# Kernel tuning notes

Hardware: AMD Instinct MI355X
Metric: run time of the kernel (lower is better)

The kernel has to match this reference:

```python
import jax, jax.numpy as jnp
import numpy as np

B, S, D, H = 32, 512, 256, 4
DK = D // H  # d_k = d_q = d_v = 64


def setup_inputs() -> dict:
    key = jax.random.key(0)
    ks = jax.random.split(key, 10)
    lim_qk = np.sqrt(6.0 / (D + DK))  # xavier_uniform for [DK, D] linears
    lim_h = np.sqrt(6.0 / (DK + D))
    return {
        "q": jax.random.normal(ks[0], (B, S, D), jnp.float32),
        "k": jax.random.normal(ks[1], (B, S, D), jnp.float32),
        "v": jax.random.normal(ks[2], (B, S, D), jnp.float32),
        # causal mask: True where attention is disallowed (masked_fill -inf)
        "mask": jnp.triu(jnp.ones((1, S, S), bool), k=1),
        # per-head query/key projections, stacked over heads: [H, DK, D]
        "Wq": jax.random.uniform(ks[3], (H, DK, D), jnp.float32, -lim_qk, lim_qk),
        "bq": jnp.zeros((H, DK), jnp.float32),
        "Wk": jax.random.uniform(ks[4], (H, DK, D), jnp.float32, -lim_qk, lim_qk),
        "bk": jnp.zeros((H, DK), jnp.float32),
        # shared value projection: [DK, D]
        "Wv": jax.random.uniform(ks[5], (DK, D), jnp.float32, -lim_qk, lim_qk),
        "bv": jnp.zeros((DK,), jnp.float32),
        # output head projection (no bias): [D, DK]
        "Wh": jax.random.uniform(ks[6], (D, DK), jnp.float32, -lim_h, lim_h),
    }


def reference(q, k, v, mask, Wq, bq, Wk, bk, Wv, bv, Wh):
    # shared V projection: [B, S, DK]
    vs = jnp.einsum("bsd,kd->bsk", v, Wv) + bv
    # per-head Q/K projections, batched over heads: [B, H, S, DK]
    qs = jnp.einsum("bsd,hkd->bhsk", q, Wq) + bq[None, :, None, :]
    ksp = jnp.einsum("bsd,hkd->bhsk", k, Wk) + bk[None, :, None, :]
    scale = jnp.sqrt(jnp.asarray(DK, jnp.float32))
    scores = jnp.einsum("bhsk,bhtk->bhst", qs, ksp) / scale  # [B, H, S, S]
    scores = jnp.where(mask[:, None, :, :], -jnp.inf, scores)
    attn = jax.nn.softmax(scores, axis=-1)  # [B, H, S, S]
    heads = jnp.einsum("bhst,btk->bhsk", attn, vs)  # [B, H, S, DK]
    out = jnp.mean(heads, axis=1)  # mean over heads -> [B, S, DK]
    out = jnp.einsum("bsk,dk->bsd", out, Wh)  # [B, S, D]
    # torch stacks attns at dim=2 -> [B, S, H, S]
    return out, jnp.transpose(attn, (0, 2, 1, 3))
```

## Files before the change

### kernel.cpp

```cpp
#include <hip/hip_runtime.h>
#include <math.h>

#define B_  32
#define S_  512
#define D_  256
#define H_  4
#define DK_ 64

typedef float  f32x4 __attribute__((ext_vector_type(4)));
typedef short  s16x8 __attribute__((ext_vector_type(8)));
typedef unsigned short u16x4 __attribute__((ext_vector_type(4)));
typedef unsigned int   u32x2 __attribute__((ext_vector_type(2)));
typedef unsigned int   u32x4 __attribute__((ext_vector_type(4)));

#define MFMA_BF16(a, b, c) __builtin_amdgcn_mfma_f32_16x16x32_bf16((a), (b), (c), 0, 0, 0)
#define GLOAD_LDS16(g, l)                                                      \
  __builtin_amdgcn_global_load_lds(                                            \
      (const __attribute__((address_space(1))) void*)(g),                      \
      (__attribute__((address_space(3))) void*)(l), 16, 0, 0)

#if __has_builtin(__builtin_amdgcn_exp2f)
#define EXP2(x) __builtin_amdgcn_exp2f(x)
#else
#define EXP2(x) __expf((x) * 0.6931471805599453f)
#endif

#define QSCALE 0.18033688011112042f

__device__ __forceinline__ unsigned short f2bf(float x) {
  unsigned int u = __float_as_uint(x);
  unsigned int r = (u + 0x7FFFu + ((u >> 16) & 1u)) >> 16;
  return (unsigned short)r;
}

__device__ __forceinline__ float bf2f(unsigned short u) {
  return __uint_as_float((unsigned int)u << 16);
}

__device__ __forceinline__ unsigned cvtpk(float lo, float hi) {
  unsigned r;
  asm("v_cvt_pk_bf16_f32 %0, %1, %2" : "=v"(r) : "v"(lo), "v"(hi));
  return r;
}

__device__ __forceinline__ s16x8 cvt8(const float* p) {
  float4 a = *(const float4*)p;
  float4 b = *(const float4*)(p + 4);
  s16x8 r;
  r[0] = (short)f2bf(a.x); r[1] = (short)f2bf(a.y);
  r[2] = (short)f2bf(a.z); r[3] = (short)f2bf(a.w);
  r[4] = (short)f2bf(b.x); r[5] = (short)f2bf(b.y);
  r[6] = (short)f2bf(b.z); r[7] = (short)f2bf(b.w);
  return r;
}

__global__ void wconv_kernel(const float* __restrict__ Wq, const float* __restrict__ Wk,
                             const float* __restrict__ Wv, const float* __restrict__ Wh,
                             unsigned short* __restrict__ out) {
  int i = blockIdx.x * 256 + threadIdx.x;
  float v, sc = 1.f;
  if (i < 65536)        { v = Wq[i];          sc = QSCALE; }
  else if (i < 131072)  { v = Wk[i - 65536]; }
  else if (i < 147456)  { v = Wv[i - 131072]; }
  else                  { v = Wh[i - 147456]; sc = 0.25f; }
  out[i] = f2bf(v * sc);
}

__global__ __launch_bounds__(256) void proj_kernel(
    const float* __restrict__ q, const float* __restrict__ k, const float* __restrict__ v,
    const unsigned short* __restrict__ Wb,
    const float* __restrict__ bq, const float* __restrict__ bk, const float* __restrict__ bv,
    unsigned short* __restrict__ qs, unsigned short* __restrict__ ks,
    unsigned short* __restrict__ vst) {
  const int y = blockIdx.y;
  const int m0 = blockIdx.x * 64;
  const int b = m0 >> 9, s0 = m0 & (S_ - 1);
  const int tid = threadIdx.x, w = tid >> 6, l = tid & 63;
  const int lr = l & 15, lg = l >> 4;
  const float* src = (y == 0) ? q : (y == 1) ? k : v;
  const float* abase = src + (size_t)(m0 + w * 16 + lr) * D_;

  __shared__ __align__(16) unsigned short Wsl[16384];

  const int nrows = (y < 2) ? 256 : 64;
  const unsigned short* wbase = Wb + (size_t)(y * 256) * D_;

  auto stW = [&](int k0) {
    const int nbytes = nrows * 128;
    for (int p = tid * 16; p < nbytes; p += 4096) {
      int row = p >> 7, c = (p >> 4) & 7;
      GLOAD_LDS16((const char*)(wbase + (size_t)row * D_ + k0) + ((c ^ (row & 7)) << 4),
                  (char*)Wsl + p);
    }
  };
  auto WF = [&](int row, int c) -> s16x8 {
    return *(const s16x8*)((const char*)Wsl + row * 128 + ((c ^ (row & 7)) << 4));
  };

  if (y < 2) {
    f32x4 acc[4][4] = {};
    for (int k0 = 0; k0 < D_; k0 += 64) {
      stW(k0);
      s16x8 af0 = cvt8(abase + k0 + 8 * lg);
      s16x8 af1 = cvt8(abase + k0 + 32 + 8 * lg);
      __syncthreads();
#pragma unroll
      for (int h = 0; h < 4; ++h) {
#pragma unroll
        for (int ns = 0; ns < 4; ++ns) {
          s16x8 wf0 = WF(h * 64 + ns * 16 + lr, lg);
          s16x8 wf1 = WF(h * 64 + ns * 16 + lr, 4 + lg);
          acc[h][ns] = MFMA_BF16(af0, wf0, acc[h][ns]);
          acc[h][ns] = MFMA_BF16(af1, wf1, acc[h][ns]);
        }
      }
      __syncthreads();
    }
    const float* bias = (y == 0) ? bq : bk;
    const float bsc = (y == 0) ? QSCALE : 1.f;
    unsigned short* dst = (y == 0) ? qs : ks;
#pragma unroll
    for (int h = 0; h < 4; ++h) {
#pragma unroll
      for (int ns = 0; ns < 4; ++ns) {
        int dk = ns * 16 + lr;
        float bb = bias[h * 64 + dk] * bsc;
#pragma unroll
        for (int i = 0; i < 4; ++i) {
          int s = s0 + w * 16 + lg * 4 + i;
          dst[(((size_t)b * H_ + h) * S_ + s) * DK_ + dk] = f2bf(acc[h][ns][i] + bb);
        }
      }
    }
  } else {
    f32x4 acc[4] = {};
    for (int k0 = 0; k0 < D_; k0 += 64) {
      stW(k0);
      s16x8 af0 = cvt8(abase + k0 + 8 * lg);
      s16x8 af1 = cvt8(abase + k0 + 32 + 8 * lg);
      __syncthreads();
#pragma unroll
      for (int ns = 0; ns < 4; ++ns) {
        s16x8 wf0 = WF(ns * 16 + lr, lg);
        s16x8 wf1 = WF(ns * 16 + lr, 4 + lg);
        acc[ns] = MFMA_BF16(af0, wf0, acc[ns]);
        acc[ns] = MFMA_BF16(af1, wf1, acc[ns]);
      }
      __syncthreads();
    }
#pragma unroll
    for (int ns = 0; ns < 4; ++ns) {
      int dk = ns * 16 + lr;
      float bb = bv[dk];
      u16x4 pk;
#pragma unroll
      for (int i = 0; i < 4; ++i) pk[i] = f2bf(acc[ns][i] + bb);
      int t = s0 + w * 16 + lg * 4;
      *(u16x4*)(vst + ((size_t)b * DK_ + dk) * S_ + t) = pk;
    }
  }
}

__global__ __launch_bounds__(512) void attn_kernel(
    const unsigned short* __restrict__ qs, const unsigned short* __restrict__ ks,
    const unsigned short* __restrict__ vst, float* __restrict__ attn,
    unsigned short* __restrict__ hh) {
  const int m = blockIdx.x;
  const int half = m >> 8, g = (m >> 1) & 1;
  const int stp = half ? (3 - g) : g;
  const int rem = ((m >> 2) & 63) * 2 + (m & 1);
  const int b = rem & 31, h = rem >> 5;
  const int tid = threadIdx.x, w = tid >> 6, l = tid & 63;
  const int lr = l & 15, lg = l >> 4;
  const int S0 = stp * 128;
  const int dtile = 2 * stp + (w >> 2);
  const int NT = 2 * stp + 2;
  const int sg = S0 + w * 16 + lr;

  __shared__ __align__(16) unsigned short Kb[2][4096];
  __shared__ __align__(16) unsigned short Vb[2][4096];
  __shared__ __align__(16) unsigned short Pb[8][16][72];

  const unsigned short* qb = qs + ((size_t)b * H_ + h) * S_ * DK_;
  const char* kbase = (const char*)(ks + ((size_t)b * H_ + h) * S_ * DK_);
  const char* vbase = (const char*)(vst + (size_t)b * DK_ * S_);

  auto stK = [&](int buf, int t0) {
    int p = tid * 16;
    int row = p >> 7, c = (p >> 4) & 7;
    GLOAD_LDS16(kbase + (size_t)t0 * 128 + row * 128 + ((c ^ (row & 7)) << 4),
                (char*)&Kb[buf][0] + p);
  };
  auto stV = [&](int buf, int t0) {
    int p = tid * 16;
    int row = p >> 7, c = (p >> 4) & 7;
    GLOAD_LDS16(vbase + (size_t)row * 1024 + t0 * 2 + ((c ^ (row & 7)) << 4),
                (char*)&Vb[buf][0] + p);
  };
  auto KF = [&](int buf, int row, int c) -> s16x8 {
    return *(const s16x8*)((const char*)&Kb[buf][0] + row * 128 + ((c ^ (row & 7)) << 4));
  };
  auto VF = [&](int buf, int row, int c) -> s16x8 {
    return *(const s16x8*)((const char*)&Vb[buf][0] + row * 128 + ((c ^ (row & 7)) << 4));
  };

  s16x8 qf0 = *(const s16x8*)(qb + (size_t)sg * DK_ + 8 * lg);
  s16x8 qf1 = *(const s16x8*)(qb + (size_t)sg * DK_ + 32 + 8 * lg);

  float ls[4] = {0.f, 0.f, 0.f, 0.f};

  stK(0, 0);
  __syncthreads();
  for (int tt = 0; tt < NT; ++tt) {
    const int cur = tt & 1;
    if (tt + 1 < NT) stK(cur ^ 1, tt * 64 + 64);
    if (tt <= dtile) {
#pragma unroll
      for (int ts = 0; ts < 4; ++ts) {
        s16x8 kf0 = KF(cur, ts * 16 + lr, lg);
        s16x8 kf1 = KF(cur, ts * 16 + lr, 4 + lg);
        f32x4 acc = {};
        acc = MFMA_BF16(kf0, qf0, acc);
        acc = MFMA_BF16(kf1, qf1, acc);
        if (tt == dtile) {
          int tb = tt * 64 + ts * 16 + 4 * lg;
#pragma unroll
          for (int i = 0; i < 4; ++i) ls[ts] += EXP2((tb + i > sg) ? -1e30f : acc[i]);
        } else {
#pragma unroll
          for (int i = 0; i < 4; ++i) ls[ts] += EXP2(acc[i]);
        }
      }
    }
    __syncthreads();
  }
  float lsum = (ls[0] + ls[1]) + (ls[2] + ls[3]);
  lsum += __shfl_xor(lsum, 16);
  lsum += __shfl_xor(lsum, 32);
  const float lg2s = __log2f(lsum);

  stK(0, 0);
  stV(0, 0);
  __syncthreads();
  f32x4 oacc[4] = {};
  for (int tt = 0; tt < NT; ++tt) {
    const int t0 = tt * 64;
    const int cur = tt & 1;
    if (tt + 1 < NT) { stK(cur ^ 1, t0 + 64); stV(cur ^ 1, t0 + 64); }
    if (tt <= dtile) {
#pragma unroll
      for (int ts = 0; ts < 4; ++ts) {
        s16x8 kf0 = KF(cur, ts * 16 + lr, lg);
        s16x8 kf1 = KF(cur, ts * 16 + lr, 4 + lg);
        f32x4 acc = {};
        acc = MFMA_BF16(kf0, qf0, acc);
        acc = MFMA_BF16(kf1, qf1, acc);
        const int tb = t0 + ts * 16 + 4 * lg;
        f32x4 p;
        if (tt == dtile) {
#pragma unroll
          for (int i = 0; i < 4; ++i)
            p[i] = EXP2(((tb + i > sg) ? -1e30f : acc[i]) - lg2s);
        } else {
#pragma unroll
          for (int i = 0; i < 4; ++i) p[i] = EXP2(acc[i] - lg2s);
        }
        *(f32x4*)(attn + (((size_t)b * S_ + sg) * H_ + h) * S_ + tb) = p;
        u32x2 pk2;
        pk2[0] = cvtpk(p[0], p[1]);
        pk2[1] = cvtpk(p[2], p[3]);
        *(u32x2*)&Pb[w][lr][ts * 16 + 4 * lg] = pk2;
      }
      asm volatile("s_waitcnt lgkmcnt(0)" ::: "memory");
      __builtin_amdgcn_sched_barrier(0);
      s16x8 pa0 = *(const s16x8*)(&Pb[w][lr][8 * lg]);
      s16x8 pa1 = *(const s16x8*)(&Pb[w][lr][32 + 8 * lg]);
#pragma unroll
      for (int ds = 0; ds < 4; ++ds) {
        s16x8 vf0 = VF(cur, ds * 16 + lr, lg);
        s16x8 vf1 = VF(cur, ds * 16 + lr, 4 + lg);
        oacc[ds] = MFMA_BF16(pa0, vf0, oacc[ds]);
        oacc[ds] = MFMA_BF16(pa1, vf1, oacc[ds]);
      }
    }
    __syncthreads();
  }

  for (int tt = dtile + 1; tt < 8; ++tt) {
    const int t0 = tt * 64;
    f32x4 z = {};
#pragma unroll
    for (int i = 0; i < 4; ++i) {
      int sr = S0 + w * 16 + lg * 4 + i;
      *(f32x4*)(attn + (((size_t)b * S_ + sr) * H_ + h) * S_ + t0 + lr * 4) = z;
    }
  }

#pragma unroll
  for (int ds = 0; ds < 4; ++ds) {
#pragma unroll
    for (int i = 0; i < 4; ++i) {
      int s = S0 + w * 16 + lg * 4 + i;
      hh[(((size_t)b * H_ + h) * S_ + s) * DK_ + ds * 16 + lr] = f2bf(oacc[ds][i]);
    }
  }
}

__global__ __launch_bounds__(256) void houtproj_kernel(
    const unsigned short* __restrict__ hh, const unsigned short* __restrict__ Whb,
    float* __restrict__ out) {
  const int m0 = blockIdx.x * 64, n0 = blockIdx.y * 64;
  const int tid = threadIdx.x, w = tid >> 6, l = tid & 63;
  const int lr = l & 15, lg = l >> 4;
  const int row = m0 + w * 16 + lr;
  const int b = row >> 9, s = row & (S_ - 1);

  __shared__ __align__(16) unsigned short Whs[4096];

#pragma unroll
  for (int it = 0; it < 2; ++it) {
    int p = it * 4096 + tid * 16;
    int r = p >> 7, c = (p >> 4) & 7;
    GLOAD_LDS16((const char*)(Whb + (size_t)(n0 + r) * DK_) + ((c ^ (r & 7)) << 4),
                (char*)Whs + p);
  }

  s16x8 af[2];
#pragma unroll
  for (int kk = 0; kk < 2; ++kk) {
    float sum8[8] = {};
#pragma unroll
    for (int hd = 0; hd < 4; ++hd) {
      s16x8 x = *(const s16x8*)(hh + (((size_t)b * H_ + hd) * S_ + s) * DK_ + kk * 32 + 8 * lg);
#pragma unroll
      for (int e = 0; e < 8; ++e) sum8[e] += bf2f((unsigned short)x[e]);
    }
    u32x4 pk;
#pragma unroll
    for (int j = 0; j < 4; ++j) pk[j] = cvtpk(sum8[2 * j], sum8[2 * j + 1]);
    af[kk] = *(s16x8*)&pk;
  }
  __syncthreads();

  auto WHF = [&](int r, int c) -> s16x8 {
    return *(const s16x8*)((const char*)Whs + r * 128 + ((c ^ (r & 7)) << 4));
  };
  f32x4 acc[4] = {};
#pragma unroll
  for (int ns = 0; ns < 4; ++ns) {
    s16x8 wf0 = WHF(ns * 16 + lr, lg);
    s16x8 wf1 = WHF(ns * 16 + lr, 4 + lg);
    acc[ns] = MFMA_BF16(af[0], wf0, acc[ns]);
    acc[ns] = MFMA_BF16(af[1], wf1, acc[ns]);
  }
#pragma unroll
  for (int ns = 0; ns < 4; ++ns) {
#pragma unroll
    for (int i = 0; i < 4; ++i) {
      out[(size_t)(m0 + w * 16 + lg * 4 + i) * D_ + n0 + ns * 16 + lr] = acc[ns][i];
    }
  }
}

extern "C" void kernel_launch(void* const* d_in, const int* in_sizes, int n_in,
                              void* d_out, int out_size, void* d_ws, size_t ws_size,
                              hipStream_t stream) {
  (void)in_sizes; (void)n_in; (void)out_size; (void)ws_size;
  const float* q  = (const float*)d_in[0];
  const float* k  = (const float*)d_in[1];
  const float* v  = (const float*)d_in[2];
  const float* Wq = (const float*)d_in[4];
  const float* bq = (const float*)d_in[5];
  const float* Wk = (const float*)d_in[6];
  const float* bk = (const float*)d_in[7];
  const float* Wv = (const float*)d_in[8];
  const float* bv = (const float*)d_in[9];
  const float* Wh = (const float*)d_in[10];

  float* out  = (float*)d_out;
  float* attn = out + (size_t)B_ * S_ * D_;

  char* ws = (char*)d_ws;
  unsigned short* Wb  = (unsigned short*)ws;
  unsigned short* qs  = (unsigned short*)(ws + 327680);
  unsigned short* ksp = (unsigned short*)(ws + 327680 + 8388608);
  unsigned short* vst = (unsigned short*)(ws + 327680 + 16777216);
  unsigned short* hh  = (unsigned short*)(ws + 327680 + 18874368);

  wconv_kernel<<<640, 256, 0, stream>>>(Wq, Wk, Wv, Wh, Wb);
  proj_kernel<<<dim3(256, 3), 256, 0, stream>>>(q, k, v, Wb, bq, bk, bv, qs, ksp, vst);
  attn_kernel<<<512, 512, 0, stream>>>(qs, ksp, vst, attn, hh);
  houtproj_kernel<<<dim3(256, 4), 256, 0, stream>>>(hh, Wb + 147456, out);
}
```

Before: 63.20 us.

## Fuse softmax normalization pass into single pass with register-held probabilities

Drops the separate first pass over K that computed the softmax row sum. A single pass now computes unnormalized exponentials, accumulates the row sum and feeds P·V, while keeping bf16-packed probabilities in registers. After the loop it writes the normalized attention map and scales the head output by the inverse sum. This removes a full QK^T recompute and its K tile loads. In exchange it holds 64 extra registers per thread, fully unrolls the tile loop, and writes attention probabilities that have been rounded to bf16 instead of kept in fp32.

```diff
diff --git a/kernel.cpp b/kernel.cpp
--- a/kernel.cpp
+++ b/kernel.cpp
@@ -208,42 +208,15 @@
   s16x8 qf1 = *(const s16x8*)(qb + (size_t)sg * DK_ + 32 + 8 * lg);
 
   float ls[4] = {0.f, 0.f, 0.f, 0.f};
-
-  stK(0, 0);
-  __syncthreads();
-  for (int tt = 0; tt < NT; ++tt) {
-    const int cur = tt & 1;
-    if (tt + 1 < NT) stK(cur ^ 1, tt * 64 + 64);
-    if (tt <= dtile) {
-#pragma unroll
-      for (int ts = 0; ts < 4; ++ts) {
-        s16x8 kf0 = KF(cur, ts * 16 + lr, lg);
-        s16x8 kf1 = KF(cur, ts * 16 + lr, 4 + lg);
-        f32x4 acc = {};
-        acc = MFMA_BF16(kf0, qf0, acc);
-        acc = MFMA_BF16(kf1, qf1, acc);
-        if (tt == dtile) {
-          int tb = tt * 64 + ts * 16 + 4 * lg;
-#pragma unroll
-          for (int i = 0; i < 4; ++i) ls[ts] += EXP2((tb + i > sg) ? -1e30f : acc[i]);
-        } else {
-#pragma unroll
-          for (int i = 0; i < 4; ++i) ls[ts] += EXP2(acc[i]);
-        }
-      }
-    }
-    __syncthreads();
-  }
-  float lsum = (ls[0] + ls[1]) + (ls[2] + ls[3]);
-  lsum += __shfl_xor(lsum, 16);
-  lsum += __shfl_xor(lsum, 32);
-  const float lg2s = __log2f(lsum);
+  unsigned preg[8][8];
+  f32x4 oacc[4] = {};
 
   stK(0, 0);
   stV(0, 0);
   __syncthreads();
-  f32x4 oacc[4] = {};
-  for (int tt = 0; tt < NT; ++tt) {
+#pragma unroll
+  for (int tt = 0; tt < 8; ++tt) {
+    if (tt >= NT) continue;
     const int t0 = tt * 64;
     const int cur = tt & 1;
     if (tt + 1 < NT) { stK(cur ^ 1, t0 + 64); stV(cur ^ 1, t0 + 64); }
@@ -256,20 +229,20 @@
         acc = MFMA_BF16(kf0, qf0, acc);
         acc = MFMA_BF16(kf1, qf1, acc);
         const int tb = t0 + ts * 16 + 4 * lg;
-        f32x4 p;
+        float p[4];
         if (tt == dtile) {
 #pragma unroll
-          for (int i = 0; i < 4; ++i)
-            p[i] = EXP2(((tb + i > sg) ? -1e30f : acc[i]) - lg2s);
+          for (int i = 0; i < 4; ++i) p[i] = EXP2((tb + i > sg) ? -1e30f : acc[i]);
         } else {
 #pragma unroll
-          for (int i = 0; i < 4; ++i) p[i] = EXP2(acc[i] - lg2s);
+          for (int i = 0; i < 4; ++i) p[i] = EXP2(acc[i]);
         }
-        *(f32x4*)(attn + (((size_t)b * S_ + sg) * H_ + h) * S_ + tb) = p;
-        u32x2 pk2;
-        pk2[0] = cvtpk(p[0], p[1]);
-        pk2[1] = cvtpk(p[2], p[3]);
-        *(u32x2*)&Pb[w][lr][ts * 16 + 4 * lg] = pk2;
+        ls[ts] += (p[0] + p[1]) + (p[2] + p[3]);
+        unsigned pk0 = cvtpk(p[0], p[1]);
+        unsigned pk1 = cvtpk(p[2], p[3]);
+        preg[tt][ts * 2] = pk0;
+        preg[tt][ts * 2 + 1] = pk1;
+        *(u32x2*)&Pb[w][lr][ts * 16 + 4 * lg] = *(u32x2*)&preg[tt][ts * 2];
       }
       asm volatile("s_waitcnt lgkmcnt(0)" ::: "memory");
       __builtin_amdgcn_sched_barrier(0);
@@ -286,6 +259,29 @@
     __syncthreads();
   }
 
+  float lsum = (ls[0] + ls[1]) + (ls[2] + ls[3]);
+  lsum += __shfl_xor(lsum, 16);
+  lsum += __shfl_xor(lsum, 32);
+  const float inv = 1.0f / lsum;
+
+#pragma unroll
+  for (int tt = 0; tt < 8; ++tt) {
+    if (tt <= dtile) {
+      const int t0 = tt * 64;
+#pragma unroll
+      for (int ts = 0; ts < 4; ++ts) {
+        unsigned a = preg[tt][ts * 2], c2 = preg[tt][ts * 2 + 1];
+        f32x4 p;
+        p[0] = bf2f((unsigned short)a) * inv;
+        p[1] = bf2f((unsigned short)(a >> 16)) * inv;
+        p[2] = bf2f((unsigned short)c2) * inv;
+        p[3] = bf2f((unsigned short)(c2 >> 16)) * inv;
+        const int tb = t0 + ts * 16 + 4 * lg;
+        *(f32x4*)(attn + (((size_t)b * S_ + sg) * H_ + h) * S_ + tb) = p;
+      }
+    }
+  }
+
   for (int tt = dtile + 1; tt < 8; ++tt) {
     const int t0 = tt * 64;
     f32x4 z = {};
@@ -296,12 +292,15 @@
     }
   }
 
+  float invO[4];
+#pragma unroll
+  for (int i = 0; i < 4; ++i) invO[i] = __shfl(inv, lg * 4 + i);
 #pragma unroll
   for (int ds = 0; ds < 4; ++ds) {
 #pragma unroll
     for (int i = 0; i < 4; ++i) {
       int s = S0 + w * 16 + lg * 4 + i;
-      hh[(((size_t)b * H_ + h) * S_ + s) * DK_ + ds * 16 + lr] = f2bf(oacc[ds][i]);
+      hh[(((size_t)b * H_ + h) * S_ + s) * DK_ + ds * 16 + lr] = f2bf(oacc[ds][i] * invO[i]);
     }
   }
 }
```

Result: no change. 62.20 us (-1.6%).
